# Kernel optimization log

Measured on AMD Instinct MI355X. Metric: run time of the kernel, lower is better.

## Reference

```python
import jax, jax.numpy as jnp
import numpy as np

NUM_MODALS = 4
SHARED_IDX = 3  # forward always uses adapter index 3 as the shared LoRA

def setup_inputs() -> dict:
    key = jax.random.key(0)
    k1, k2, k3, k4, k5 = jax.random.split(key, 5)
    M, B, n, c, r = NUM_MODALS, 8, 1024, 768, 16
    x = jax.random.normal(k1, (M * B, n, c), dtype=jnp.float32)
    Wp = jax.random.normal(k2, (c, c), dtype=jnp.float32) * 0.02   # proj weight [out,in]
    bp = jax.random.normal(k3, (c,), dtype=jnp.float32) * 0.02     # proj bias
    A = jax.random.normal(k4, (M, r, c), dtype=jnp.float32) * 0.02  # linear_a_o weights [r,c]
    Bw = jax.random.normal(k5, (M, c, r), dtype=jnp.float32) * 0.02 # linear_b_o weights [c,r]
    return {"x": x, "Wp": Wp, "bp": bp, "A": A, "Bw": Bw}

def reference(x, Wp, bp, A, Bw):
    bs_m, n, c = x.shape
    xm = x.reshape(NUM_MODALS, -1, n, c)  # [M,B,n,c]
    # base projection (dense GEMM) + bias
    base = jnp.einsum('mbnc,oc->mbno', xm, Wp) + bp
    # shared LoRA (adapter index 3 for every modality)
    sh_lo = jnp.einsum('mbnc,rc->mbnr', xm, A[SHARED_IDX])
    shared = jnp.einsum('mbnr,or->mbno', sh_lo, Bw[SHARED_IDX])
    # modality-specific LoRA (batched over modality axis)
    sp_lo = jnp.einsum('mbnc,mrc->mbnr', xm, A)
    specific = jnp.einsum('mbnr,mor->mbno', sp_lo, Bw)
    out = base + shared + specific
    return out.reshape(bs_m, n, -1)
```

## Files before the change

### kernel.cpp

```cpp
#include <hip/hip_runtime.h>
#include <hip/hip_bf16.h>
#include <stdint.h>

#define NUM_MODALS 4
#define SHARED_IDX 3

typedef __attribute__((ext_vector_type(8))) short bf16x8;
typedef __attribute__((ext_vector_type(4))) float floatx4;

__device__ __forceinline__ unsigned short f2bf(float f) {
  unsigned int u = __float_as_uint(f);
  u += 0x7fffu + ((u >> 16) & 1u);
  return (unsigned short)(u >> 16);
}

__global__ __launch_bounds__(256) void weff_fast(
    const float* __restrict__ Wp, const float* __restrict__ A,
    const float* __restrict__ Bw, unsigned short* __restrict__ Weff) {
  const int c  = blockIdx.x * 256 + threadIdx.x;
  const int o0 = blockIdx.y * 16;
  const int m  = blockIdx.z;

  __shared__ float b3[256], bm[256];
  const int t = threadIdx.x;
  {
    const int o = o0 + (t >> 4);
    const int r = t & 15;
    b3[t] = Bw[(SHARED_IDX * 768 + o) * 16 + r];
    bm[t] = Bw[((size_t)m * 768 + o) * 16 + r];
  }
  __syncthreads();

  float a3[16], am[16];
#pragma unroll
  for (int r = 0; r < 16; ++r) {
    a3[r] = A[(SHARED_IDX * 16 + r) * 768 + c];
    am[r] = A[((size_t)m * 16 + r) * 768 + c];
  }
#pragma unroll 4
  for (int oo = 0; oo < 16; ++oo) {
    const int o = o0 + oo;
    float acc = Wp[(size_t)o * 768 + c];
#pragma unroll
    for (int r = 0; r < 16; ++r) {
      acc += b3[oo * 16 + r] * a3[r];
      acc += bm[oo * 16 + r] * am[r];
    }
    Weff[((size_t)m * 768 + o) * 768 + c] = f2bf(acc);
  }
}

__global__ __launch_bounds__(256) void lora_gemm_fused(
    const float* __restrict__ X,
    const unsigned short* __restrict__ Weff,
    const float* __restrict__ bp,
    float* __restrict__ out) {
  const int bid = blockIdx.x;
  const int xcd = bid & 7;
  const int s   = bid >> 3;
  const int w   = xcd * 192 + s;
  const int ct  = w % 6;
  const int rt  = w / 6;
  const int m        = rt >> 6;
  const int row_base = (rt & 63) * 128;
  const int col_base = ct * 128;

  __shared__ alignas(16) unsigned short As[2 * 128 * 64];
  __shared__ alignas(16) unsigned short Ws[2 * 128 * 64];

  const int tid  = threadIdx.x;
  const int wave = tid >> 6;
  const int lane = tid & 63;
  const int ln = lane & 15;
  const int qd = lane >> 4;
  const int wm = wave & 1;
  const int wn = wave >> 1;

  const float*          Xm = X    + (size_t)m * 8192 * 768;
  const unsigned short* Wm = Weff + (size_t)m * 768 * 768;

  floatx4 acc[4][4];
#pragma unroll
  for (int i = 0; i < 4; ++i)
#pragma unroll
    for (int j = 0; j < 4; ++j)
      acc[i][j] = (floatx4)(0.0f);

  const int xr   = tid >> 4;
  const int xc   = (tid & 15) * 4;
  const int cb   = xc >> 3;
  const int half = (xc >> 2) & 1;
  const float* xsrc[8];
  unsigned short* xdst[8];
#pragma unroll
  for (int p = 0; p < 8; ++p) {
    const int r = xr + p * 16;
    xsrc[p] = Xm + (size_t)(row_base + r) * 768 + xc;
    xdst[p] = &As[r * 64 + (cb ^ (r & 7)) * 8 + half * 4];
  }
  const int sr = lane >> 3;
  const int ss = lane & 7;
  const unsigned short* wsrc[4];
#pragma unroll
  for (int p = 0; p < 4; ++p) {
    const int r = wave * 32 + p * 8 + sr;
    wsrc[p] = Wm + (size_t)(col_base + r) * 768 + (ss ^ (r & 7)) * 8;
  }

  float4 xv[8];
#pragma unroll
  for (int p = 0; p < 8; ++p) {
    xv[p] = *(const float4*)xsrc[p];
    xsrc[p] += 64;
  }
#pragma unroll
  for (int p = 0; p < 4; ++p) {
    __builtin_amdgcn_global_load_lds(
        (const __attribute__((address_space(1))) void*)wsrc[p],
        (__attribute__((address_space(3))) void*)&Ws[(wave * 32 + p * 8) * 64],
        16, 0, 0);
    wsrc[p] += 64;
  }

  for (int kt = 0; kt < 12; ++kt) {
    const int boff = (kt & 1) * (128 * 64);

#pragma unroll
    for (int p = 0; p < 8; ++p) {
      const float4 v = xv[p];
      __hip_bfloat162 h0 = __float22bfloat162_rn(make_float2(v.x, v.y));
      __hip_bfloat162 h1 = __float22bfloat162_rn(make_float2(v.z, v.w));
      uint2 hv;
      hv.x = *(unsigned int*)&h0;
      hv.y = *(unsigned int*)&h1;
      *(uint2*)(xdst[p] + boff) = hv;
    }

    __syncthreads();

    if (kt < 11) {
      const int nboff = boff ^ (128 * 64);
#pragma unroll
      for (int p = 0; p < 8; ++p) {
        xv[p] = *(const float4*)xsrc[p];
        xsrc[p] += 64;
      }
#pragma unroll
      for (int p = 0; p < 4; ++p) {
        __builtin_amdgcn_global_load_lds(
            (const __attribute__((address_space(1))) void*)wsrc[p],
            (__attribute__((address_space(3))) void*)&Ws[nboff + (wave * 32 + p * 8) * 64],
            16, 0, 0);
        wsrc[p] += 64;
      }
      __builtin_amdgcn_sched_barrier(0);
    }

#pragma unroll
    for (int kk = 0; kk < 64; kk += 32) {
      const int kblk = (kk >> 3) + qd;
      const int slot = (kblk ^ (ln & 7)) * 8;
      bf16x8 a[4], b[4];
#pragma unroll
      for (int i = 0; i < 4; ++i)
        a[i] = *(const bf16x8*)(&As[boff + (wm * 64 + i * 16 + ln) * 64 + slot]);
#pragma unroll
      for (int j = 0; j < 4; ++j)
        b[j] = *(const bf16x8*)(&Ws[boff + (wn * 64 + j * 16 + ln) * 64 + slot]);
#pragma unroll
      for (int i = 0; i < 4; ++i)
#pragma unroll
        for (int j = 0; j < 4; ++j)
          acc[i][j] = __builtin_amdgcn_mfma_f32_16x16x32_bf16(a[i], b[j], acc[i][j], 0, 0, 0);
    }
  }

  float* Om = out + (size_t)m * 8192 * 768;
#pragma unroll
  for (int j = 0; j < 4; ++j) {
    const int o = col_base + wn * 64 + j * 16 + ln;
    const float bias = bp[o];
#pragma unroll
    for (int i = 0; i < 4; ++i) {
      const int R = row_base + wm * 64 + i * 16 + qd * 4;
      float* dst = Om + (size_t)R * 768 + o;
#pragma unroll
      for (int v = 0; v < 4; ++v)
        dst[(size_t)v * 768] = acc[i][j][v] + bias;
    }
  }
}

extern "C" void kernel_launch(void* const* d_in, const int* in_sizes, int n_in,
                              void* d_out, int out_size, void* d_ws, size_t ws_size,
                              hipStream_t stream) {
  const float* x  = (const float*)d_in[0];
  const float* Wp = (const float*)d_in[1];
  const float* bp = (const float*)d_in[2];
  const float* A  = (const float*)d_in[3];
  const float* Bw = (const float*)d_in[4];
  float* out = (float*)d_out;

  unsigned short* Weff = (unsigned short*)d_ws;

  weff_fast<<<dim3(3, 48, 4), 256, 0, stream>>>(Wp, A, Bw, Weff);
  lora_gemm_fused<<<dim3(1536), 256, 0, stream>>>(x, Weff, bp, out);
}
```

Baseline: 241.7 us.

## Restructure GEMM pipeline: single-buffer A, prefetch W two tiles ahead, explicit waitcnts

The X tile in LDS becomes single-buffered, with two barriers per k-step instead of one. The W tile is now prefetched two iterations ahead through global_load_lds, using explicit vmcnt waits to overlap the weight load with compute. s_setprio is raised around the MFMA block. The aim is better latency hiding and less LDS use, which may raise occupancy, at the cost of an extra barrier per iteration and fragile hand-counted vmcnt values.

Result: faster. 232.6 us (-3.8%).

```diff
diff --git a/kernel.cpp b/kernel.cpp
--- a/kernel.cpp
+++ b/kernel.cpp
@@ -65,7 +65,7 @@
   const int row_base = (rt & 63) * 128;
   const int col_base = ct * 128;
 
-  __shared__ alignas(16) unsigned short As[2 * 128 * 64];
+  __shared__ alignas(16) unsigned short As[128 * 64];
   __shared__ alignas(16) unsigned short Ws[2 * 128 * 64];
 
   const int tid  = threadIdx.x;
@@ -109,11 +109,6 @@
 
   float4 xv[8];
 #pragma unroll
-  for (int p = 0; p < 8; ++p) {
-    xv[p] = *(const float4*)xsrc[p];
-    xsrc[p] += 64;
-  }
-#pragma unroll
   for (int p = 0; p < 4; ++p) {
     __builtin_amdgcn_global_load_lds(
         (const __attribute__((address_space(1))) void*)wsrc[p],
@@ -121,9 +116,28 @@
         16, 0, 0);
     wsrc[p] += 64;
   }
+#pragma unroll
+  for (int p = 0; p < 8; ++p) {
+    xv[p] = *(const float4*)xsrc[p];
+    xsrc[p] += 64;
+  }
+#pragma unroll
+  for (int p = 0; p < 4; ++p) {
+    __builtin_amdgcn_global_load_lds(
+        (const __attribute__((address_space(1))) void*)wsrc[p],
+        (__attribute__((address_space(3))) void*)&Ws[128 * 64 + (wave * 32 + p * 8) * 64],
+        16, 0, 0);
+    wsrc[p] += 64;
+  }
 
   for (int kt = 0; kt < 12; ++kt) {
     const int boff = (kt & 1) * (128 * 64);
+
+    if (kt < 11) {
+      asm volatile("s_waitcnt vmcnt(4)" ::: "memory");
+    } else {
+      asm volatile("s_waitcnt vmcnt(0)" ::: "memory");
+    }
 
 #pragma unroll
     for (int p = 0; p < 8; ++p) {
@@ -133,29 +147,23 @@
       uint2 hv;
       hv.x = *(unsigned int*)&h0;
       hv.y = *(unsigned int*)&h1;
-      *(uint2*)(xdst[p] + boff) = hv;
-    }
-
-    __syncthreads();
+      *(uint2*)xdst[p] = hv;
+    }
 
     if (kt < 11) {
-      const int nboff = boff ^ (128 * 64);
 #pragma unroll
       for (int p = 0; p < 8; ++p) {
         xv[p] = *(const float4*)xsrc[p];
         xsrc[p] += 64;
       }
-#pragma unroll
-      for (int p = 0; p < 4; ++p) {
-        __builtin_amdgcn_global_load_lds(
-            (const __attribute__((address_space(1))) void*)wsrc[p],
-            (__attribute__((address_space(3))) void*)&Ws[nboff + (wave * 32 + p * 8) * 64],
-            16, 0, 0);
-        wsrc[p] += 64;
-      }
-      __builtin_amdgcn_sched_barrier(0);
-    }
-
+    }
+
+    asm volatile("s_waitcnt lgkmcnt(0)" ::: "memory");
+    __builtin_amdgcn_sched_barrier(0);
+    __builtin_amdgcn_s_barrier();
+    __builtin_amdgcn_sched_barrier(0);
+
+    __builtin_amdgcn_s_setprio(1);
 #pragma unroll
     for (int kk = 0; kk < 64; kk += 32) {
       const int kblk = (kk >> 3) + qd;
@@ -163,7 +171,7 @@
       bf16x8 a[4], b[4];
 #pragma unroll
       for (int i = 0; i < 4; ++i)
-        a[i] = *(const bf16x8*)(&As[boff + (wm * 64 + i * 16 + ln) * 64 + slot]);
+        a[i] = *(const bf16x8*)(&As[(wm * 64 + i * 16 + ln) * 64 + slot]);
 #pragma unroll
       for (int j = 0; j < 4; ++j)
         b[j] = *(const bf16x8*)(&Ws[boff + (wn * 64 + j * 16 + ln) * 64 + slot]);
@@ -172,6 +180,22 @@
 #pragma unroll
         for (int j = 0; j < 4; ++j)
           acc[i][j] = __builtin_amdgcn_mfma_f32_16x16x32_bf16(a[i], b[j], acc[i][j], 0, 0, 0);
+    }
+    __builtin_amdgcn_s_setprio(0);
+
+    __builtin_amdgcn_sched_barrier(0);
+    __builtin_amdgcn_s_barrier();
+    __builtin_amdgcn_sched_barrier(0);
+
+    if (kt < 10) {
+#pragma unroll
+      for (int p = 0; p < 4; ++p) {
+        __builtin_amdgcn_global_load_lds(
+            (const __attribute__((address_space(1))) void*)wsrc[p],
+            (__attribute__((address_space(3))) void*)&Ws[boff + (wave * 32 + p * 8) * 64],
+            16, 0, 0);
+        wsrc[p] += 64;
+      }
     }
   }
 
```
